# Optimization experiments

Measured on AMD Instinct MI355X. Metric: run time of the kernel, lower is better.

Reference implementation:

```python
import jax, jax.numpy as jnp
import numpy as np

SUB_NO = 20
T_NO = 201
E_NO = 2000
I_NO = 500
T_DATA = 20000

def _make_cden():
    C = np.zeros((SUB_NO, SUB_NO), dtype=np.float32)
    for i in range(SUB_NO):
        for c in (2 * i + 1, 2 * i + 2):
            if c < SUB_NO:
                C[i, c] = 1.0
    return C

C_DEN = _make_cden()
CHILDREN = [np.where(C_DEN[s] == 1)[0] for s in range(SUB_NO)]  # static tree structure


def setup_inputs() -> dict:
    key = jax.random.key(0)
    ks = jax.random.split(key, 12)
    eps = 1e-6
    inp = {}
    inp['S_e'] = jax.random.uniform(ks[0], (T_DATA, E_NO), dtype=jnp.float32)
    inp['S_i'] = jax.random.uniform(ks[1], (T_DATA, I_NO), dtype=jnp.float32)
    # uniform noise for REBAR reparam; clipped away from {0,1} so log(-log(u)) is finite
    inp['u'] = jnp.clip(jax.random.uniform(ks[2], (SUB_NO, E_NO + I_NO), dtype=jnp.float32), eps, 1.0 - eps)
    inp['v'] = jnp.clip(jax.random.uniform(ks[3], (SUB_NO, E_NO + I_NO), dtype=jnp.float32), eps, 1.0 - eps)
    inp['W_syn'] = jax.random.normal(ks[4], (SUB_NO, 2), dtype=jnp.float32) * 0.1
    inp['Tau_syn'] = jnp.ones((SUB_NO, 2), dtype=jnp.float32)
    inp['Delta_syn'] = jax.random.uniform(ks[5], (SUB_NO, 2), dtype=jnp.float32)
    inp['W_sub'] = jax.random.uniform(ks[6], (SUB_NO,), dtype=jnp.float32)
    inp['V_o'] = jax.random.normal(ks[7], (1,), dtype=jnp.float32)
    inp['Theta'] = jnp.zeros((SUB_NO,), dtype=jnp.float32)
    inp['C_syn_log'] = jnp.ones((SUB_NO, E_NO + I_NO), dtype=jnp.float32)
    return inp


def _H(x):
    # one-hot of per-column argmax (first max, as torch.argmax)
    idx = jnp.argmax(x, axis=0)
    return jax.nn.one_hot(idx, x.shape[0], axis=0, dtype=x.dtype)


def _reparam_pz(u, theta):
    return jnp.log(theta) - jnp.log(-jnp.log(u))


def _reparam_pz_b(v, b, theta):
    # b is one-hot per column; v_k = v at the b==1 row of each column
    v_k = jnp.sum(v * b, axis=0, keepdims=True)  # [1, cols]
    z_same = -jnp.log(-jnp.log(v))
    z_diff = -jnp.log(-jnp.log(v) / theta - jnp.log(v_k))
    return b * z_same + (1.0 - b) * z_diff


def _evaluate_f(C_syn, S_e, S_i, W_syn, Tau_syn, Delta_syn, W_sub, V_o):
    T_data = S_e.shape[0]
    C_syn_e = C_syn[:, :E_NO]          # [sub, E]
    C_syn_i = C_syn[:, -I_NO:]         # [sub, I]
    # double-exponential (alpha) synaptic kernels, vectorized over subunits & e/i
    t_raw = jnp.arange(T_NO, dtype=S_e.dtype)                               # [T_no]
    t = jnp.maximum(t_raw[None, None, :] - jnp.exp(Delta_syn)[:, :, None], 0.0)  # [sub,2,T_no]
    t_tau = t / jnp.exp(Tau_syn)[:, :, None]
    kern = t_tau * jnp.exp(-t_tau) * W_syn[:, :, None]                      # [sub,2,T_no]
    # project spikes onto subunits
    in_e = S_e @ C_syn_e.T   # [T, sub]
    in_i = S_i @ C_syn_i.T   # [T, sub]
    # causal depthwise conv: syn[t,s] = sum_tau kern[s,:,tau] * in[t-tau,s]
    inp = jnp.stack([in_e.T, in_i.T], axis=1).reshape(1, SUB_NO * 2, T_data)   # NCH
    k = jnp.flip(kern, axis=-1).reshape(SUB_NO * 2, 1, T_NO)                   # OIH
    filt = jax.lax.conv_general_dilated(
        inp, k, window_strides=(1,), padding=[(T_NO - 1, 0)],
        feature_group_count=SUB_NO * 2,
        dimension_numbers=('NCH', 'OIH', 'NCH'))
    syn_in = filt.reshape(SUB_NO, 2, T_data).sum(axis=1).T   # [T, sub]
    # tree-recurrent tanh aggregation (children have higher index than parents)
    sub_out = [None] * SUB_NO
    for s in range(SUB_NO):
        idx = SUB_NO - 1 - s
        ch = CHILDREN[idx]
        if ch.size == 0:
            sub_out[idx] = jnp.tanh(syn_in[:, idx])
        else:
            leaf = sum(sub_out[c] * W_sub[c] for c in ch)
            sub_out[idx] = jnp.tanh(syn_in[:, idx] + leaf)
    return sub_out[0] * W_sub[0] + V_o[0]


def reference(S_e, S_i, u, v, W_syn, Tau_syn, Delta_syn, W_sub, V_o, Theta, C_syn_log):
    theta = jax.nn.softmax(C_syn_log, axis=0)
    rebar_z = _reparam_pz(u, theta)
    hard_z = _H(rebar_z)
    rebar_zb = _reparam_pz_b(v, hard_z, theta)
    soft_z = jax.nn.sigmoid(rebar_z / 0.5) + 1e-9
    soft_zb = jax.nn.sigmoid(rebar_zb / 0.5) + 1e-9
    V_hard_z = _evaluate_f(hard_z, S_e, S_i, W_syn, Tau_syn, Delta_syn, W_sub, V_o)
    V_soft_z = _evaluate_f(soft_z, S_e, S_i, W_syn, Tau_syn, Delta_syn, W_sub, V_o)
    V_soft_zb = _evaluate_f(soft_zb, S_e, S_i, W_syn, Tau_syn, Delta_syn, W_sub, V_o)
    return (V_hard_z, V_soft_z, V_soft_zb, theta, hard_z, soft_z, soft_zb)
```

## Files before the change

kernel.cpp:

```cpp
#include <hip/hip_runtime.h>
#include <math.h>

#define SUBS 20
#define TAPS 201
#define ENO 2000
#define INO 500
#define TDATA 20000

typedef __bf16 bf16x8 __attribute__((ext_vector_type(8)));
typedef float f32x4 __attribute__((ext_vector_type(4)));

#define WGE_STRIDE 2048
#define WGI_STRIDE 512

#define WGE_OFF  0ull
#define WGI_OFF  262144ull
#define KERN_OFF 327680ull
#define INE_OFF  360448ull
#define INI_OFF  (INE_OFF + 4800000ull)
#define P1_OFF   (INI_OFF + 4800000ull)
#define P2_OFF   (P1_OFF  + 4800000ull)
#define P3_OFF   (P2_OFF  + 4800000ull)
#define SYN_OFF  (P3_OFF  + 4800000ull)

__device__ __forceinline__ unsigned short f2bf(float f) {
  union { float f; unsigned int u; } c; c.f = f;
  unsigned int u = c.u;
  return (unsigned short)((u + 0x7FFFu + ((u >> 16) & 1u)) >> 16);
}

__device__ __forceinline__ float fast_tanh(float x) {
  const float ax = fabsf(x);
  const float e  = __expf(2.f * ax);
  const float t  = 1.f - 2.f / (e + 1.f);
  return copysignf(t, x);
}

__global__ __launch_bounds__(256) void prep_kernel(
    const float* __restrict__ u, const float* __restrict__ v,
    const float* __restrict__ C_log, const float* __restrict__ W_syn,
    const float* __restrict__ Tau_syn, const float* __restrict__ Delta_syn,
    float* __restrict__ out,
    unsigned short* __restrict__ wge, unsigned short* __restrict__ wgi,
    float* __restrict__ kern)
{
  if (blockIdx.x < 10) {
    const int n = blockIdx.x * 256 + threadIdx.x;
    if (n >= 2500) return;
    float x[SUBS], theta[SUBS], rebar[SUBS];
    float mx = -1e30f;
#pragma unroll
    for (int s = 0; s < SUBS; ++s) { x[s] = C_log[s*2500 + n]; mx = fmaxf(mx, x[s]); }
    float sum = 0.f;
#pragma unroll
    for (int s = 0; s < SUBS; ++s) { theta[s] = __expf(x[s] - mx); sum += theta[s]; }
    const float inv = 1.f / sum;
    int idx = 0; float best = -1e30f;
#pragma unroll
    for (int s = 0; s < SUBS; ++s) {
      theta[s] *= inv;
      out[60000 + s*2500 + n] = theta[s];
      const float uu = u[s*2500 + n];
      const float r = __logf(theta[s]) - __logf(-__logf(uu));
      rebar[s] = r;
      if (r > best) { best = r; idx = s; }
    }
    const float lvk = __logf(v[idx*2500 + n]);
#pragma unroll
    for (int s = 0; s < SUBS; ++s) {
      const float hz = (s == idx) ? 1.f : 0.f;
      const float sz = 1.f / (1.f + __expf(-2.f * rebar[s])) + 1e-9f;
      const float vv = v[s*2500 + n];
      const float zb = (s == idx) ? (-__logf(-__logf(vv)))
                                  : (-__logf(-__logf(vv) / theta[s] - lvk));
      const float szb = 1.f / (1.f + __expf(-2.f * zb)) + 1e-9f;
      out[110000 + s*2500 + n] = hz;
      out[160000 + s*2500 + n] = sz;
      out[210000 + s*2500 + n] = szb;
      if (n < ENO) {
        wge[(s     )*WGE_STRIDE + n] = f2bf(hz);
        wge[(20 + s)*WGE_STRIDE + n] = f2bf(sz);
        wge[(40 + s)*WGE_STRIDE + n] = f2bf(szb);
      } else {
        const int k = n - ENO;
        wgi[(s     )*WGI_STRIDE + k] = f2bf(hz);
        wgi[(20 + s)*WGI_STRIDE + k] = f2bf(sz);
        wgi[(40 + s)*WGI_STRIDE + k] = f2bf(szb);
      }
    }
  } else {
    const int tid = threadIdx.x;
    for (int i = tid; i < 40*TAPS; i += 256) {
      const int ch = i / TAPS, m = i - ch*TAPS;
      const float dl  = __expf(Delta_syn[ch]);
      const float tau = __expf(Tau_syn[ch]);
      const float t  = fmaxf((float)m - dl, 0.f);
      const float tt = t / tau;
      kern[i] = tt * __expf(-tt) * W_syn[ch];
    }
    for (int i = tid; i < 4*2048; i += 256) wge[(60 + (i >> 11))*WGE_STRIDE + (i & 2047)] = 0;
    for (int i = tid; i < 60*48;  i += 256) wge[(i / 48)*WGE_STRIDE + 2000 + (i % 48)] = 0;
    for (int i = tid; i < 4*512;  i += 256) wgi[(60 + (i >> 9))*WGI_STRIDE + (i & 511)] = 0;
    for (int i = tid; i < 60*12;  i += 256) wgi[(i / 12)*WGI_STRIDE + 500 + (i % 12)] = 0;
  }
}

__global__ __launch_bounds__(256) void gemm_kernel(
    const float* __restrict__ S_e, const float* __restrict__ S_i,
    const unsigned short* __restrict__ wge, const unsigned short* __restrict__ wgi,
    float* __restrict__ in_e, float* __restrict__ in_i,
    float* __restrict__ P1, float* __restrict__ P2, float* __restrict__ P3)
{
  const int tid  = threadIdx.x;
  const int wave = tid >> 6;
  const int lane = tid & 63;
  const int m16  = lane & 15;
  const int quad = lane >> 4;
  const int t0   = blockIdx.x * 64;
  const int cy   = blockIdx.y;
  const bool isE = (cy < 4);

  const float* S = isE ? S_e : S_i;
  const unsigned short* Wg = isE ? wge : wgi;
  float* outp = (cy == 0) ? in_e : (cy == 1) ? P1 : (cy == 2) ? P2
              : (cy == 3) ? P3   : in_i;
  const int K       = isE ? ENO : INO;
  const int Wstride = isE ? WGE_STRIDE : WGI_STRIDE;
  const int k_base  = isE ? cy * 512 : 0;

  const int tA = t0 + wave*16 + m16;
  const float* Arow = S + (size_t)((tA < TDATA) ? tA : TDATA - 1) * K;
  const unsigned short* B0 = Wg + (size_t)(m16     ) * Wstride;
  const unsigned short* B1 = Wg + (size_t)(m16 + 16) * Wstride;
  const unsigned short* B2 = Wg + (size_t)(m16 + 32) * Wstride;
  const unsigned short* B3 = Wg + (size_t)(m16 + 48) * Wstride;

  f32x4 acc0 = {0.f,0.f,0.f,0.f};
  f32x4 acc1 = acc0, acc2 = acc0, acc3 = acc0;

#pragma unroll
  for (int st = 0; st < 8; ++st) {
#pragma unroll
    for (int h = 0; h < 2; ++h) {
      const int kh = k_base + st*64 + h*32 + quad*8;
      const int c0 = (kh + 4 <= K) ? kh     : K - 4;
      const int c1 = (kh + 8 <= K) ? kh + 4 : K - 4;
      const float4 va = *(const float4*)(Arow + c0);
      const float4 vb = *(const float4*)(Arow + c1);
      const bf16x8 b0 = *(const bf16x8*)(B0 + kh);
      const bf16x8 b1 = *(const bf16x8*)(B1 + kh);
      const bf16x8 b2 = *(const bf16x8*)(B2 + kh);
      const bf16x8 b3 = *(const bf16x8*)(B3 + kh);
      bf16x8 a;
      a[0] = (__bf16)va.x; a[1] = (__bf16)va.y;
      a[2] = (__bf16)va.z; a[3] = (__bf16)va.w;
      a[4] = (__bf16)vb.x; a[5] = (__bf16)vb.y;
      a[6] = (__bf16)vb.z; a[7] = (__bf16)vb.w;
      acc0 = __builtin_amdgcn_mfma_f32_16x16x32_bf16(a, b0, acc0, 0, 0, 0);
      acc1 = __builtin_amdgcn_mfma_f32_16x16x32_bf16(a, b1, acc1, 0, 0, 0);
      acc2 = __builtin_amdgcn_mfma_f32_16x16x32_bf16(a, b2, acc2, 0, 0, 0);
      acc3 = __builtin_amdgcn_mfma_f32_16x16x32_bf16(a, b3, acc3, 0, 0, 0);
    }
  }

  const int t = t0 + wave*16 + quad*4;
  if (t < TDATA) {
    float* o = outp + t;
    *(float4*)(o + (size_t)(     m16)*TDATA) = *(float4*)&acc0;
    *(float4*)(o + (size_t)(16 + m16)*TDATA) = *(float4*)&acc1;
    *(float4*)(o + (size_t)(32 + m16)*TDATA) = *(float4*)&acc2;
    if (m16 < 12)
      *(float4*)(o + (size_t)(48 + m16)*TDATA) = *(float4*)&acc3;
  }
}

__device__ __forceinline__ int swz(int i) { return i + (i >> 5); }

__global__ __launch_bounds__(256) void conv_kernel(
    const float* __restrict__ in_e, const float* __restrict__ P1,
    const float* __restrict__ P2,  const float* __restrict__ P3,
    const float* __restrict__ in_i,
    const float* __restrict__ kern, float* __restrict__ syn)
{
  __shared__ float Ee[2320];
  __shared__ float Ei[2320];
  const int ch = blockIdx.y;
  const int t0 = blockIdx.x * 2048;
  const int s  = ch % SUBS;
  const size_t off = (size_t)ch * TDATA;
  for (int i = threadIdx.x; i < 2248; i += 256) {
    const int g = t0 - 200 + i;
    float e = 0.f, ii = 0.f;
    if (g >= 0 && g < TDATA) {
      e = in_e[off + g] + P1[off + g] + P2[off + g] + P3[off + g];
      ii = in_i[off + g];
    }
    Ee[swz(i)] = e;
    Ei[swz(i)] = ii;
  }
  __syncthreads();
  const float* ke = kern + (size_t)(s*2    ) * TAPS;
  const float* ki = kern + (size_t)(s*2 + 1) * TAPS;
  const int tb = threadIdx.x * 8;
  float acc[8] = {0.f,0.f,0.f,0.f,0.f,0.f,0.f,0.f};
  float we[8], wi[8];
#pragma unroll
  for (int j = 0; j < 8; ++j) {
    we[j] = Ee[swz(tb + 200 + j)];
    wi[j] = Ei[swz(tb + 200 + j)];
  }
#pragma unroll 8
  for (int m = 0; m < TAPS; ++m) {
    const float k0 = ke[m];
    const float k1 = ki[m];
#pragma unroll
    for (int j = 0; j < 8; ++j)
      acc[j] = fmaf(we[j], k0, fmaf(wi[j], k1, acc[j]));
    if (m < TAPS - 1) {
#pragma unroll
      for (int j = 7; j > 0; --j) { we[j] = we[j-1]; wi[j] = wi[j-1]; }
      we[0] = Ee[swz(tb + 199 - m)];
      wi[0] = Ei[swz(tb + 199 - m)];
    }
  }
  const int t = t0 + tb;
  if (t < TDATA) {
    float* o = syn + off + t;
    *(float4*)(o    ) = make_float4(acc[0], acc[1], acc[2], acc[3]);
    *(float4*)(o + 4) = make_float4(acc[4], acc[5], acc[6], acc[7]);
  }
}

__global__ __launch_bounds__(256) void tree_kernel(
    const float* __restrict__ syn, const float* __restrict__ W_sub,
    const float* __restrict__ V_o, float* __restrict__ out)
{
  const int t = blockIdx.x * 256 + threadIdx.x;
  const int var = blockIdx.y;
  if (t >= TDATA) return;
  const float* sp = syn + (size_t)var * SUBS * TDATA + t;
  float so[SUBS];
#pragma unroll
  for (int s = SUBS - 1; s >= 0; --s) {
    float val = sp[(size_t)s * TDATA];
    const int c1 = 2*s + 1, c2 = 2*s + 2;
    if (c1 < SUBS) val += so[c1] * W_sub[c1];
    if (c2 < SUBS) val += so[c2] * W_sub[c2];
    so[s] = fast_tanh(val);
  }
  out[(size_t)var * TDATA + t] = so[0] * W_sub[0] + V_o[0];
}

extern "C" void kernel_launch(void* const* d_in, const int* in_sizes, int n_in,
                              void* d_out, int out_size, void* d_ws, size_t ws_size,
                              hipStream_t stream) {
  const float* S_e     = (const float*)d_in[0];
  const float* S_i     = (const float*)d_in[1];
  const float* u       = (const float*)d_in[2];
  const float* v       = (const float*)d_in[3];
  const float* W_syn   = (const float*)d_in[4];
  const float* Tau_syn = (const float*)d_in[5];
  const float* Delta   = (const float*)d_in[6];
  const float* W_sub   = (const float*)d_in[7];
  const float* V_o     = (const float*)d_in[8];
  const float* C_log   = (const float*)d_in[10];
  float* out = (float*)d_out;
  char* ws = (char*)d_ws;
  unsigned short* wge = (unsigned short*)(ws + WGE_OFF);
  unsigned short* wgi = (unsigned short*)(ws + WGI_OFF);
  float* kern = (float*)(ws + KERN_OFF);
  float* in_e = (float*)(ws + INE_OFF);
  float* in_i = (float*)(ws + INI_OFF);
  float* P1   = (float*)(ws + P1_OFF);
  float* P2   = (float*)(ws + P2_OFF);
  float* P3   = (float*)(ws + P3_OFF);
  float* syn  = (float*)(ws + SYN_OFF);

  prep_kernel<<<dim3(11), dim3(256), 0, stream>>>(u, v, C_log, W_syn, Tau_syn,
                                                  Delta, out, wge, wgi, kern);
  gemm_kernel<<<dim3(313, 5), dim3(256), 0, stream>>>(
      S_e, S_i, wge, wgi, in_e, in_i, P1, P2, P3);
  conv_kernel<<<dim3(10, 60), dim3(256), 0, stream>>>(in_e, P1, P2, P3, in_i,
                                                      kern, syn);
  tree_kernel<<<dim3(79, 3), dim3(256), 0, stream>>>(syn, W_sub, V_o, out);
}
```

Baseline: 346.6 us.

## Stage A tiles through per-wave double-buffered LDS with coalesced loads and prefetch

The GEMM kernel no longer has each lane load two strided float4 pieces of S straight into MFMA fragments. Each wave now loads its 16x64 A slice with a coalesced layout (4 lanes per row, 16 floats each), converts it to bf16 and writes it to a padded, double-buffered LDS tile. The global load for the next k-step is issued before the MFMAs of the current step, so the loads overlap with compute. This costs LDS traffic and more registers, and it relies on wave-local LDS ordering with no explicit barrier.

After: 346.8 us. Within noise of the previous version (+0.1%).

```diff
diff --git a/kernel.cpp b/kernel.cpp
--- a/kernel.cpp
+++ b/kernel.cpp
@@ -111,11 +111,14 @@
     float* __restrict__ in_e, float* __restrict__ in_i,
     float* __restrict__ P1, float* __restrict__ P2, float* __restrict__ P3)
 {
+  __shared__ unsigned short Alds[4][2][16*72];
   const int tid  = threadIdx.x;
   const int wave = tid >> 6;
   const int lane = tid & 63;
   const int m16  = lane & 15;
   const int quad = lane >> 4;
+  const int rr   = lane >> 2;
+  const int s4   = lane & 3;
   const int t0   = blockIdx.x * 64;
   const int cy   = blockIdx.y;
   const bool isE = (cy < 4);
@@ -128,8 +131,9 @@
   const int Wstride = isE ? WGE_STRIDE : WGI_STRIDE;
   const int k_base  = isE ? cy * 512 : 0;
 
-  const int tA = t0 + wave*16 + m16;
+  const int tA = t0 + wave*16 + rr;
   const float* Arow = S + (size_t)((tA < TDATA) ? tA : TDATA - 1) * K;
+
   const unsigned short* B0 = Wg + (size_t)(m16     ) * Wstride;
   const unsigned short* B1 = Wg + (size_t)(m16 + 16) * Wstride;
   const unsigned short* B2 = Wg + (size_t)(m16 + 32) * Wstride;
@@ -138,30 +142,59 @@
   f32x4 acc0 = {0.f,0.f,0.f,0.f};
   f32x4 acc1 = acc0, acc2 = acc0, acc3 = acc0;
 
+#define LDA(st, d0, d1, d2, d3) do {                                  \
+    const int cb_ = k_base + (st)*64 + s4*4;                          \
+    const int c0_ = (cb_      <= K-4) ? cb_      : K-4;               \
+    const int c1_ = (cb_ + 16 <= K-4) ? cb_ + 16 : K-4;               \
+    const int c2_ = (cb_ + 32 <= K-4) ? cb_ + 32 : K-4;               \
+    const int c3_ = (cb_ + 48 <= K-4) ? cb_ + 48 : K-4;               \
+    d0 = *(const float4*)(Arow + c0_);                                \
+    d1 = *(const float4*)(Arow + c1_);                                \
+    d2 = *(const float4*)(Arow + c2_);                                \
+    d3 = *(const float4*)(Arow + c3_);                                \
+  } while (0)
+
+#define STW(d, f0_, f1_, f2_, f3_) do {                               \
+    unsigned short* w_ = &Alds[wave][d][rr*72 + s4*4];                \
+    ushort4 q_;                                                       \
+    q_.x=f2bf(f0_.x); q_.y=f2bf(f0_.y); q_.z=f2bf(f0_.z); q_.w=f2bf(f0_.w); \
+    *(ushort4*)(w_     ) = q_;                                        \
+    q_.x=f2bf(f1_.x); q_.y=f2bf(f1_.y); q_.z=f2bf(f1_.z); q_.w=f2bf(f1_.w); \
+    *(ushort4*)(w_ + 16) = q_;                                        \
+    q_.x=f2bf(f2_.x); q_.y=f2bf(f2_.y); q_.z=f2bf(f2_.z); q_.w=f2bf(f2_.w); \
+    *(ushort4*)(w_ + 32) = q_;                                        \
+    q_.x=f2bf(f3_.x); q_.y=f2bf(f3_.y); q_.z=f2bf(f3_.z); q_.w=f2bf(f3_.w); \
+    *(ushort4*)(w_ + 48) = q_;                                        \
+  } while (0)
+
+  {
+    float4 f0, f1, f2, f3;
+    LDA(0, f0, f1, f2, f3);
+    STW(0, f0, f1, f2, f3);
+  }
+
 #pragma unroll
   for (int st = 0; st < 8; ++st) {
+    float4 n0, n1, n2, n3;
+    if (st < 7) LDA(st + 1, n0, n1, n2, n3);
+    const unsigned short* bufc = &Alds[wave][st & 1][0];
 #pragma unroll
     for (int h = 0; h < 2; ++h) {
       const int kh = k_base + st*64 + h*32 + quad*8;
-      const int c0 = (kh + 4 <= K) ? kh     : K - 4;
-      const int c1 = (kh + 8 <= K) ? kh + 4 : K - 4;
-      const float4 va = *(const float4*)(Arow + c0);
-      const float4 vb = *(const float4*)(Arow + c1);
       const bf16x8 b0 = *(const bf16x8*)(B0 + kh);
       const bf16x8 b1 = *(const bf16x8*)(B1 + kh);
       const bf16x8 b2 = *(const bf16x8*)(B2 + kh);
       const bf16x8 b3 = *(const bf16x8*)(B3 + kh);
-      bf16x8 a;
-      a[0] = (__bf16)va.x; a[1] = (__bf16)va.y;
-      a[2] = (__bf16)va.z; a[3] = (__bf16)va.w;
-      a[4] = (__bf16)vb.x; a[5] = (__bf16)vb.y;
-      a[6] = (__bf16)vb.z; a[7] = (__bf16)vb.w;
+      const bf16x8 a  = *(const bf16x8*)(bufc + m16*72 + h*32 + quad*8);
       acc0 = __builtin_amdgcn_mfma_f32_16x16x32_bf16(a, b0, acc0, 0, 0, 0);
       acc1 = __builtin_amdgcn_mfma_f32_16x16x32_bf16(a, b1, acc1, 0, 0, 0);
       acc2 = __builtin_amdgcn_mfma_f32_16x16x32_bf16(a, b2, acc2, 0, 0, 0);
       acc3 = __builtin_amdgcn_mfma_f32_16x16x32_bf16(a, b3, acc3, 0, 0, 0);
     }
-  }
+    if (st < 7) STW((st + 1) & 1, n0, n1, n2, n3);
+  }
+#undef LDA
+#undef STW
 
   const int t = t0 + wave*16 + quad*4;
   if (t < TDATA) {
```
